# Kernel optimization log

Hardware: AMD Instinct MI355X
Metric: run time of the kernel (lower is better)

Reference implementation:

```python
import jax, jax.numpy as jnp
import numpy as np

STRIDES = (128, 64, 32, 16, 8)
FM_SHAPES = ((6, 10), (12, 20), (24, 40), (48, 80), (96, 160))
RATIOS = np.array([1.0, 2.0, 3.0])
BASE_SIZE = 4
POS_THR, NEG_THR, IGNORE = 0.5, 0.4, -1.0
ALPHA, GAMMA, SIGMA = 0.25, 2.0, 3.0


def _cell_anchors(stride):
    # classic generate_anchors: base 4x4 anchor, 3 aspect ratios, scale=stride
    w = h = float(BASE_SIZE)
    ctr = (BASE_SIZE - 1) / 2.0
    size = w * h
    ws = np.round(np.sqrt(size / RATIOS))
    hs = np.round(ws * RATIOS)
    a = np.stack([ctr - 0.5 * (ws - 1), ctr - 0.5 * (hs - 1),
                  ctr + 0.5 * (ws - 1), ctr + 0.5 * (hs - 1)], 1)
    aw = a[:, 2] - a[:, 0] + 1
    ah = a[:, 3] - a[:, 1] + 1
    cx = a[:, 0] + 0.5 * (aw - 1)
    cy = a[:, 1] + 0.5 * (ah - 1)
    sw = aw * stride
    sh = ah * stride
    return np.stack([cx - 0.5 * (sw - 1), cy - 0.5 * (sh - 1),
                     cx + 0.5 * (sw - 1), cy + 0.5 * (sh - 1)], 1)


def _all_anchors():
    outs = []
    for (h, w), s in zip(FM_SHAPES, STRIDES):
        cell = _cell_anchors(s)  # [3,4]
        sx = np.tile((np.arange(w) * s)[None, :], (h, 1)).reshape(-1)
        sy = np.tile((np.arange(h) * s)[:, None], (1, w)).reshape(-1)
        shifts = np.stack([sx, sy, sx, sy], 1)  # [h*w,4]
        outs.append((cell[None] + shifts[:, None]).reshape(-1, 4))
    return np.concatenate(outs, 0).astype(np.float32)  # [A,4]


def box_overlap(b, g):
    ab = (b[:, 2] - b[:, 0] + 1) * (b[:, 3] - b[:, 1] + 1)
    ag = (g[:, 2] - g[:, 0] + 1) * (g[:, 3] - g[:, 1] + 1)
    iw = jnp.clip(jnp.minimum(b[:, None, 2], g[None, :, 2]) - jnp.maximum(b[:, None, 0], g[None, :, 0]) + 1, 0)
    ih = jnp.clip(jnp.minimum(b[:, None, 3], g[None, :, 3]) - jnp.maximum(b[:, None, 1], g[None, :, 1]) + 1, 0)
    inter = iw * ih
    return inter / (ab[:, None] + ag[None, :] - inter)


def bbox_transform_inv(anc, dlt):
    w = anc[..., 2] - anc[..., 0] + 1
    h = anc[..., 3] - anc[..., 1] + 1
    cx = anc[..., 0] + 0.5 * (w - 1)
    cy = anc[..., 1] + 0.5 * (h - 1)
    mx = jnp.log(jnp.asarray(1000.0 / 16, dlt.dtype))
    pw = jnp.exp(jnp.minimum(dlt[..., 2], mx)) * w
    ph = jnp.exp(jnp.minimum(dlt[..., 3], mx)) * h
    pcx = dlt[..., 0] * w + cx
    pcy = dlt[..., 1] * h + cy
    return jnp.stack([pcx - 0.5 * (pw - 1), pcy - 0.5 * (ph - 1),
                      pcx + 0.5 * (pw - 1), pcy + 0.5 * (ph - 1)], -1)


def bbox_transform(anc, gt):
    aw = anc[..., 2] - anc[..., 0] + 1
    ah = anc[..., 3] - anc[..., 1] + 1
    acx = anc[..., 0] + 0.5 * (aw - 1)
    acy = anc[..., 1] + 0.5 * (ah - 1)
    gw = gt[..., 2] - gt[..., 0] + 1
    gh = gt[..., 3] - gt[..., 1] + 1
    gcx = gt[..., 0] + 0.5 * (gw - 1)
    gcy = gt[..., 1] + 0.5 * (gh - 1)
    return jnp.stack([(gcx - acx) / aw, (gcy - acy) / ah,
                      jnp.log(gw / aw), jnp.log(gh / ah)], -1)


def conv3x3(x, w, b):
    y = jax.lax.conv_general_dilated(x, w, (1, 1), 'SAME',
                                     dimension_numbers=('NCHW', 'OIHW', 'NCHW'))
    return y + b[None, :, None, None]


def _head(feat, cls_w, cls_b, box_w, box_b, score_w, score_b,
          bpred_w, bpred_b, iou_w, iou_b, num_w, num_b):
    n = feat.shape[0]
    c = feat
    for i in range(4):
        c = jax.nn.relu(conv3x3(c, cls_w[i], cls_b[i]))
    cls_prob = jax.nn.sigmoid(conv3x3(c, score_w, score_b))
    num_prob = conv3x3(c, num_w, num_b)
    r = feat
    for i in range(4):
        r = jax.nn.relu(conv3x3(r, box_w[i], box_b[i]))
    offsets = conv3x3(r, bpred_w, bpred_b)
    iou_prob = conv3x3(r, iou_w, iou_b)
    rs = lambda t, ch: t.transpose(0, 2, 3, 1).reshape(n, -1, ch)
    return rs(cls_prob, 2), rs(num_prob, 2), rs(offsets, 8), rs(iou_prob, 2)


def _forward(feats, gt_boxes, im_info, cls_w, cls_b, box_w, box_b,
             score_w, score_b, bpred_w, bpred_b, iou_w, iou_b, num_w, num_b):
    outs = [_head(f, cls_w, cls_b, box_w, box_b, score_w, score_b,
                  bpred_w, bpred_b, iou_w, iou_b, num_w, num_b) for f in feats]
    cls_prob = jnp.concatenate([o[0] for o in outs], 1)  # [n,A,2]
    num_prob = jnp.concatenate([o[1] for o in outs], 1)  # [n,A,2]
    offsets = jnp.concatenate([o[2] for o in outs], 1)   # [n,A,8]
    iou_prob = jnp.concatenate([o[3] for o in outs], 1)  # [n,A,2]
    anchors = jnp.asarray(_all_anchors())                # [A,4]
    A = anchors.shape[0]
    n = cls_prob.shape[0]
    G = gt_boxes.shape[1]
    counts = im_info[:, 5]
    gidx = jnp.arange(G, dtype=jnp.float32)

    def anchor_target_one(gt, cnt):
        valid = (gidx < cnt) & (gt[:, 4] != IGNORE)
        ov = jnp.where(valid[None, :], box_overlap(anchors, gt[:, :4]), -1.0)
        top2, idx = jax.lax.top_k(ov, 2)  # [A,2]
        labels = jnp.where(top2 >= POS_THR, 1.0,
                           jnp.where(top2 < NEG_THR, 0.0, -1.0))
        tgt = bbox_transform(anchors[:, None, :], gt[idx, :4])  # [A,2,4]
        return labels, tgt.reshape(-1, 4)

    rpn_labels, target_boxes = jax.vmap(anchor_target_one)(gt_boxes, counts)
    rpn_labels = jax.lax.stop_gradient(rpn_labels)        # [n,A,2]
    target_boxes = jax.lax.stop_gradient(target_boxes)    # [n,2A,4]
    anchors2 = jnp.repeat(anchors, 2, axis=0)             # [2A,4] interleaved

    def iou_target_one(gt, cnt, off):
        dt = bbox_transform_inv(anchors2, off.reshape(-1, 4))  # [2A,4]
        keep = ((gidx < cnt) & (gt[:, 4] != IGNORE)).astype(dt.dtype)
        ov = box_overlap(dt, gt[:, :4]) * keep[None, :]        # [2A,G]
        ov = ov.reshape(A, 2, G)
        a, b = ov[:, 0], ov[:, 1]
        i1 = jnp.argmax(a, 1)
        av = jnp.take_along_axis(a, i1[:, None], 1)
        b = b.at[jnp.arange(A), i1].set(0.0)
        bv = jnp.max(b, 1, keepdims=True)
        return jnp.concatenate([av, bv], 1)                    # [A,2]

    ious_target = jax.lax.stop_gradient(
        jax.vmap(iou_target_one)(gt_boxes, counts, offsets))

    a, b = rpn_labels[..., 0], rpn_labels[..., 1]
    ignores = b - (a == 0).astype(b.dtype) * (b != 0).astype(b.dtype)
    labels = jnp.stack([a, ignores], 2).reshape(n, -1)     # [n,2A]

    # focal (sigmoid_cross_entropy_retina)
    p = cls_prob.reshape(n, -1, 1)                          # [n,2A,1]
    mask = (labels != IGNORE).astype(p.dtype)
    onehot = ((labels * mask) == 1).astype(p.dtype)[..., None]
    pos = (1 - p) ** GAMMA * onehot * jnp.log(p)
    neg = p ** GAMMA * (1 - onehot) * jnp.log(1 - p)
    npos = jnp.maximum((labels > 0).astype(p.dtype).sum(), 1.0)
    cls_loss = (-(ALPHA * pos + (1 - ALPHA) * neg).sum(-1) * mask).sum() / npos

    # smooth_l1_loss_retina (sigma=3)
    off4 = offsets.reshape(n, -1, 4)                        # [n,2A,4]
    diff = off4 - target_boxes
    ad = jnp.abs(diff)
    s2 = SIGMA * SIGMA
    sl1 = jnp.where(ad < 1.0 / s2, 0.5 * s2 * diff * diff, ad - 0.5 / s2)
    posm = (labels > 0).astype(off4.dtype)
    bbox_loss = (sl1.sum(-1) * posm).sum() / jnp.maximum(posm.sum(), 1.0)

    # iou_l1_loss
    lab2 = labels.reshape(n, -1, 2)                         # [n,A,2]
    ioumask = (lab2 > 0).astype(iou_prob.dtype)
    iou_loss = (jnp.abs(iou_prob.reshape(n, -1, 2) - ious_target) * ioumask).sum() \
        / jnp.maximum(ioumask.sum(), 1.0)

    # softmax_loss over num-per-anchor predictions
    nlabels = (lab2 > 0).sum(2).reshape(-1) - 1             # [n*A] in {-1,0,1}
    score = num_prob.reshape(-1, 2)
    logp = jax.nn.log_softmax(score, -1)
    nm = (nlabels != -1)
    vl = jnp.where(nm, nlabels, 0)
    nmf = nm.astype(score.dtype)
    num_loss = (-(jnp.take_along_axis(logp, vl[:, None], 1)[:, 0]) * nmf).sum() \
        / jnp.maximum(nmf.sum(), 1.0)

    return jnp.stack([cls_loss, 2.0 * bbox_loss, 2.0 * iou_loss, num_loss])


def setup_inputs() -> dict:
    key = jax.random.key(0)
    ks = jax.random.split(key, 24)
    n, G = 2, 32
    inp = {}
    for i, (h, w) in enumerate(FM_SHAPES):
        inp[f"feat_p{7 - i}"] = jax.random.normal(ks[i], (n, 256, h, w), jnp.float32) * 0.5
    x1 = jax.random.uniform(ks[5], (n, G), minval=0.0, maxval=900.0)
    y1 = jax.random.uniform(ks[6], (n, G), minval=0.0, maxval=500.0)
    bw = jax.random.uniform(ks[7], (n, G), minval=32.0, maxval=300.0)
    bh = jax.random.uniform(ks[8], (n, G), minval=32.0, maxval=300.0)
    inp["gt_boxes"] = jnp.stack([x1, y1, x1 + bw, y1 + bh, jnp.ones((n, G))], -1).astype(jnp.float32)
    inp["im_info"] = jnp.tile(jnp.array([[768., 1280., 1., 768., 1280., 24.]], jnp.float32), (n, 1))
    std = 0.01
    inp["cls_w"] = jax.random.normal(ks[9], (4, 256, 256, 3, 3), jnp.float32) * std
    inp["cls_b"] = jnp.zeros((4, 256), jnp.float32)
    inp["box_w"] = jax.random.normal(ks[10], (4, 256, 256, 3, 3), jnp.float32) * std
    inp["box_b"] = jnp.zeros((4, 256), jnp.float32)
    prior_bias = -float(np.log((1 - 0.01) / 0.01))
    inp["score_w"] = jax.random.normal(ks[11], (6, 256, 3, 3), jnp.float32) * std
    inp["score_b"] = jnp.full((6,), prior_bias, jnp.float32)
    inp["bpred_w"] = jax.random.normal(ks[12], (24, 256, 3, 3), jnp.float32) * std
    inp["bpred_b"] = jnp.zeros((24,), jnp.float32)
    inp["iou_w"] = jax.random.normal(ks[13], (6, 256, 3, 3), jnp.float32) * std
    inp["iou_b"] = jnp.zeros((6,), jnp.float32)
    inp["num_w"] = jax.random.normal(ks[14], (6, 256, 3, 3), jnp.float32) * std
    inp["num_b"] = jnp.zeros((6,), jnp.float32)
    return inp


def reference(feat_p7, feat_p6, feat_p5, feat_p4, feat_p3, gt_boxes, im_info,
              cls_w, cls_b, box_w, box_b, score_w, score_b, bpred_w, bpred_b,
              iou_w, iou_b, num_w, num_b):
    feats = [feat_p7, feat_p6, feat_p5, feat_p4, feat_p3]
    return _forward(feats, gt_boxes, im_info, cls_w, cls_b, box_w, box_b,
                    score_w, score_b, bpred_w, bpred_b, iou_w, iou_b, num_w, num_b)
```

## Files before the change

kernel.cpp:

```cpp
#include <hip/hip_runtime.h>
#include <math.h>

#define A_TOTAL 61380
#define NGT 32
#define PTOT 21472

typedef _Float16 f16;
typedef f16 f16x8 __attribute__((ext_vector_type(8)));
typedef float f32x4 __attribute__((ext_vector_type(4)));

__device__ __constant__ int LV_H[5]    = {6, 12, 24, 48, 96};
__device__ __constant__ int LV_W[5]    = {10, 20, 40, 80, 160};
__device__ __constant__ int LV_PB[5]   = {0, 96, 404, 1496, 5596};
__device__ __constant__ int LV_TX[5]   = {1, 2, 3, 5, 10};

__device__ __forceinline__ void get_tile8(int t, int& lv, int& y0, int& x0)
{
  int local;
  if (t >= 44)      { lv = 4; local = t - 44; }
  else if (t >= 14) { lv = 3; local = t - 14; }
  else if (t >= 5)  { lv = 2; local = t - 5; }
  else if (t >= 1)  { lv = 1; local = t - 1; }
  else              { lv = 0; local = 0; }
  int tX = LV_TX[lv];
  y0 = (local / tX) * 8;
  x0 = (local % tX) * 16;
}

__device__ __forceinline__ void get_tile16(int t, int& lv, int& y0, int& x0)
{
  int local;
  if (t >= 24)      { lv = 4; local = t - 24; }
  else if (t >= 9)  { lv = 3; local = t - 9; }
  else if (t >= 3)  { lv = 2; local = t - 3; }
  else if (t >= 1)  { lv = 1; local = t - 1; }
  else              { lv = 0; local = 0; }
  int tX = LV_TX[lv];
  y0 = (local / tX) * 16;
  x0 = (local % tX) * 16;
}

__device__ __forceinline__ int padded_off(int p)
{
  if (p >= 5100)      { int po = p - 5100; int y = po / 160, x = po - y * 160; return 5596 + (y + 1) * 162 + x + 1; }
  else if (p >= 1260) { int po = p - 1260; int y = po / 80,  x = po - y * 80;  return 1496 + (y + 1) * 82  + x + 1; }
  else if (p >= 300)  { int po = p - 300;  int y = po / 40,  x = po - y * 40;  return 404  + (y + 1) * 42  + x + 1; }
  else if (p >= 60)   { int po = p - 60;   int y = po / 20,  x = po - y * 20;  return 96   + (y + 1) * 22  + x + 1; }
  else                { int y = p / 10, x = p - y * 10;                         return (y + 1) * 12 + x + 1; }
}

__global__ __launch_bounds__(64) void zero_borders(f16* __restrict__ act)
{
  int e = blockIdx.x, b = blockIdx.y, z = blockIdx.z;
  int lv, e0;
  if (e >= 496)      { lv = 4; e0 = e - 496; }
  else if (e >= 236) { lv = 3; e0 = e - 236; }
  else if (e >= 104) { lv = 2; e0 = e - 104; }
  else if (e >= 36)  { lv = 1; e0 = e - 36; }
  else               { lv = 0; e0 = e; }
  int Hp = LV_H[lv] + 2, Wp = LV_W[lv] + 2;
  int y, x;
  if (e0 < Wp)          { y = 0;      x = e0; }
  else if (e0 < 2 * Wp) { y = Hp - 1; x = e0 - Wp; }
  else { int e2 = e0 - 2 * Wp; y = 1 + (e2 >> 1); x = (e2 & 1) ? (Wp - 1) : 0; }
  f16* dst = act + ((size_t)z * 2 * PTOT + (size_t)b * PTOT + LV_PB[lv] + y * Wp + x) * 256
           + threadIdx.x * 4;
  *(uint2*)dst = (uint2){0u, 0u};
}

__global__ __launch_bounds__(256) void feats_to_nhwc(
    const float* __restrict__ f0, const float* __restrict__ f1,
    const float* __restrict__ f2, const float* __restrict__ f3,
    const float* __restrict__ f4, f16* __restrict__ act)
{
  const int b = blockIdx.z;
  const int c0 = blockIdx.y * 32;
  const int p0 = blockIdx.x * 32;
  const int tx = threadIdx.x & 31, ty = threadIdx.x >> 5;
  __shared__ float tl[32][33];

  int p = p0 + tx;
  const float* src = f0; int po = 0;
  if (p >= 5100)      { src = f4; po = p - 5100; }
  else if (p >= 1260) { src = f3; po = p - 1260; }
  else if (p >= 300)  { src = f2; po = p - 300;  }
  else if (p >= 60)   { src = f1; po = p - 60;   }
  else                { src = f0; po = p;        }
  int HW = (p >= 5100) ? 15360 : (p >= 1260) ? 3840 : (p >= 300) ? 960 : (p >= 60) ? 240 : 60;

#pragma unroll
  for (int k = 0; k < 4; ++k) {
    int c = c0 + ty + k * 8;
    float v = 0.f;
    if (p < 20460) v = src[((size_t)b * 256 + c) * HW + po];
    tl[ty + k * 8][tx] = v;
  }
  __syncthreads();
#pragma unroll
  for (int k = 0; k < 4; ++k) {
    int pp = p0 + ty + k * 8;
    if (pp < 20460)
      act[((size_t)b * PTOT + padded_off(pp)) * 256 + c0 + tx] = (f16)tl[tx][ty + k * 8];
  }
}

__global__ __launch_bounds__(256) void prep_tower_w3(
    const float* __restrict__ cls_w, const float* __restrict__ box_w,
    f16* __restrict__ wT)
{
  int blk = blockIdx.x;
  int l = blk >> 8, co = blk & 255;
  const float* src = (l < 4 ? cls_w + (size_t)l * 589824
                            : box_w + (size_t)(l - 4) * 589824)
                   + (size_t)co * 2304;
  __shared__ f16 sm[2304];
  int t = threadIdx.x;
#pragma unroll
  for (int j = 0; j < 9; ++j) sm[t + j * 256] = (f16)src[t + j * 256];
  __syncthreads();
#pragma unroll
  for (int it = 0; it < 2; ++it) {
    int c = t + it * 256;
    if (c < 288) {
      int tap = c >> 5, s = c & 31;
      f16x8 v;
#pragma unroll
      for (int e = 0; e < 8; ++e) v[e] = sm[(s * 8 + e) * 9 + tap];
      *(f16x8*)(wT + ((((size_t)l * 9 + tap) * 32 + s) * 256 + co) * 8) = v;
    }
  }
}

__global__ void prep_head_w3(const float* __restrict__ sw, const float* __restrict__ nw,
                             const float* __restrict__ bw, const float* __restrict__ iw,
                             const float* __restrict__ sb, const float* __restrict__ nb2,
                             const float* __restrict__ bb, const float* __restrict__ ib,
                             f16* __restrict__ wH, float* __restrict__ hb)
{
  int idx = blockIdx.x * 256 + threadIdx.x;
  if (idx < 18432) {
    int p = idx / 9216, rem = idx - p * 9216;
    int tap = rem / 1024, rem2 = rem - tap * 1024;
    int s = rem2 >> 5, co = rem2 & 31;
    int C1 = p ? 24 : 6;
    const float* w1 = p ? bw : sw;
    const float* w2 = p ? iw : nw;
    f16x8 v;
#pragma unroll
    for (int e = 0; e < 8; ++e) {
      int ci = s * 8 + e;
      float x = 0.f;
      if (co < C1)          x = w1[((size_t)co * 256 + ci) * 9 + tap];
      else if (co < C1 + 6) x = w2[((size_t)(co - C1) * 256 + ci) * 9 + tap];
      v[e] = (f16)x;
    }
    *(f16x8*)(wH + (size_t)idx * 8) = v;
  }
  if (idx < 64) {
    int pp = idx >> 5, jj = idx & 31;
    int C1b = pp ? 24 : 6;
    const float* b1 = pp ? bb : sb;
    const float* b2 = pp ? ib : nb2;
    float bv = 0.f;
    if (jj < C1b)          bv = b1[jj];
    else if (jj < C1b + 6) bv = b2[jj - C1b];
    hb[idx] = bv;
  }
}

__global__ __launch_bounds__(256, 2) void conv_mfma_tower3(
    const f16* __restrict__ in_cls, f16* __restrict__ out_cls,
    const f16* __restrict__ in_box, f16* __restrict__ out_box,
    const f16* __restrict__ wT, const float* __restrict__ cls_b,
    const float* __restrict__ box_b, int layer)
{
  int lv, y0, x0;
  get_tile8(blockIdx.x, lv, y0, x0);
  const int H = LV_H[lv], W = LV_W[lv], Wp = W + 2, pbase = LV_PB[lv];
  const int b = blockIdx.y, tw = blockIdx.z;
  const f16* in  = tw ? in_box : in_cls;
  f16*       out = tw ? out_box : out_cls;
  const f16* wB = wT + (size_t)(tw * 4 + layer) * 2304 * 256;
  const float* bias = (tw ? box_b : cls_b) + layer * 256;

  const int tid = threadIdx.x;
  const int lane = tid & 63, wid = tid >> 6;
  const int m = lane & 15, q = lane >> 4;
  const int mrow = (wid & 1) * 4;
  const int ncol = (wid >> 1) * 128;

  f32x4 acc[4][8];
#pragma unroll
  for (int i = 0; i < 4; ++i)
#pragma unroll
    for (int j = 0; j < 8; ++j) acc[i][j] = (f32x4){0.f, 0.f, 0.f, 0.f};

  const f16* inb = in + (size_t)(b * PTOT + pbase) * 256;
  const f16* pA = inb + ((size_t)(y0 + mrow) * Wp + x0 + m) * 256 + q * 8;
  const f16* pB = wB + ((size_t)q * 256 + ncol + m) * 8;

  for (int cb = 0; cb < 8; ++cb) {
    const f16* pAc = pA + cb * 32;
    const f16* pBc = pB + (size_t)cb * 4 * 256 * 8;
#pragma unroll
    for (int tap = 0; tap < 9; ++tap) {
      const int ky = tap / 3, kx = tap - ky * 3;
      f16x8 af[4], bf[8];
#pragma unroll
      for (int mb = 0; mb < 4; ++mb)
        af[mb] = *(const f16x8*)(pAc + ((size_t)(mb + ky) * Wp + kx) * 256);
#pragma unroll
      for (int nb = 0; nb < 8; ++nb)
        bf[nb] = *(const f16x8*)(pBc + (size_t)tap * 65536 + nb * 128);
#pragma unroll
      for (int mb = 0; mb < 4; ++mb)
#pragma unroll
        for (int nb = 0; nb < 8; ++nb)
          acc[mb][nb] = __builtin_amdgcn_mfma_f32_16x16x32_f16(af[mb], bf[nb], acc[mb][nb], 0, 0, 0);
    }
  }

  f16* outb = out + (size_t)(b * PTOT + pbase) * 256;
#pragma unroll
  for (int mb = 0; mb < 4; ++mb) {
    int y = y0 + mrow + mb;
    if (y >= H) continue;
#pragma unroll
    for (int nb = 0; nb < 8; ++nb) {
      int co = ncol + nb * 16 + m;
      float bi = bias[co];
#pragma unroll
      for (int r = 0; r < 4; ++r) {
        int x = x0 + q * 4 + r;
        if (x < W) {
          float v = fmaxf(acc[mb][nb][r] + bi, 0.f);
          outb[((size_t)(y + 1) * Wp + x + 1) * 256 + co] = (f16)v;
        }
      }
    }
  }
}

__global__ __launch_bounds__(256) void conv_mfma_head3(
    const f16* __restrict__ in_cls, const f16* __restrict__ in_box,
    const f16* __restrict__ wH, const float* __restrict__ hb,
    float* __restrict__ cls_prob, float* __restrict__ num_prob,
    float* __restrict__ offsets, float* __restrict__ iou_prob)
{
  int lv, y0, x0;
  get_tile16(blockIdx.x, lv, y0, x0);
  const int H = LV_H[lv], W = LV_W[lv], Wp = W + 2, pbase = LV_PB[lv];
  const int b = blockIdx.y, z = blockIdx.z;
  const f16* in = z ? in_box : in_cls;
  const f16* wB = wH + (size_t)z * 2304 * 32;
  const float* hbz = hb + z * 32;
  float* o1 = z ? offsets : cls_prob;
  float* o2 = z ? iou_prob : num_prob;
  const int C1 = z ? 24 : 6, P1 = z ? 8 : 2, SIG = z ? 0 : 1;

  const int tid = threadIdx.x;
  const int lane = tid & 63, wid = tid >> 6;
  const int m = lane & 15, q = lane >> 4;

  f32x4 acc[4][2];
#pragma unroll
  for (int i = 0; i < 4; ++i) { acc[i][0] = (f32x4){0,0,0,0}; acc[i][1] = (f32x4){0,0,0,0}; }

  const f16* inb = in + (size_t)(b * PTOT + pbase) * 256;
  const f16* pA = inb + ((size_t)(y0 + wid * 4) * Wp + x0 + m) * 256 + q * 8;
  const f16* pB = wB + ((size_t)q * 32 + m) * 8;

  for (int cb = 0; cb < 8; ++cb) {
    const f16* pAc = pA + cb * 32;
    const f16* pBc = pB + (size_t)cb * 4 * 32 * 8;
#pragma unroll
    for (int tap = 0; tap < 9; ++tap) {
      const int ky = tap / 3, kx = tap - ky * 3;
      f16x8 af[4], bf[2];
#pragma unroll
      for (int mb = 0; mb < 4; ++mb)
        af[mb] = *(const f16x8*)(pAc + ((size_t)(mb + ky) * Wp + kx) * 256);
#pragma unroll
      for (int nb = 0; nb < 2; ++nb)
        bf[nb] = *(const f16x8*)(pBc + (size_t)tap * 8192 + nb * 128);
#pragma unroll
      for (int mb = 0; mb < 4; ++mb)
#pragma unroll
        for (int nb = 0; nb < 2; ++nb)
          acc[mb][nb] = __builtin_amdgcn_mfma_f32_16x16x32_f16(af[mb], bf[nb], acc[mb][nb], 0, 0, 0);
    }
  }

  const int ro = pbase * 0 + 0;
  const int robase = (lv == 0 ? 0 : lv == 1 ? 60 : lv == 2 ? 300 : lv == 3 ? 1260 : 5100) * 3;
#pragma unroll
  for (int mb = 0; mb < 4; ++mb) {
    int y = y0 + wid * 4 + mb;
    if (y >= H) continue;
#pragma unroll
    for (int nb = 0; nb < 2; ++nb) {
      int j = nb * 16 + m;
      if (j >= C1 + 6) continue;
      float bi = hbz[j];
#pragma unroll
      for (int r = 0; r < 4; ++r) {
        int x = x0 + q * 4 + r;
        if (x < W) {
          float v = acc[mb][nb][r] + bi;
          int row0 = robase + (y * W + x) * 3;
          if (j < C1) {
            if (SIG) v = 1.f / (1.f + expf(-v));
            int jd = j / P1;
            o1[((size_t)b * A_TOTAL + row0 + jd) * P1 + (j - jd * P1)] = v;
          } else {
            int jj = j - C1;
            o2[((size_t)b * A_TOTAL + row0 + (jj >> 1)) * 2 + (jj & 1)] = v;
          }
        }
      }
    }
  }
  (void)ro;
}

__global__ void gen_anchors(float* __restrict__ anchors, float* __restrict__ accum)
{
  int i = blockIdx.x * 256 + threadIdx.x;
  if (blockIdx.x == 0 && threadIdx.x < 8) accum[threadIdx.x] = 0.f;
  if (i >= A_TOTAL) return;
  int off, s, Wl;
  if (i >= 15300)     { off = 15300; s = 8;   Wl = 160; }
  else if (i >= 3780) { off = 3780;  s = 16;  Wl = 80;  }
  else if (i >= 900)  { off = 900;   s = 32;  Wl = 40;  }
  else if (i >= 180)  { off = 180;   s = 64;  Wl = 20;  }
  else                { off = 0;     s = 128; Wl = 10;  }
  int r = i - off;
  int cell = r / 3, a = r - cell * 3;
  int y = cell / Wl, x = cell - y * Wl;
  float wsv = (a == 0) ? 4.f : (a == 1) ? 3.f : 2.f;
  float hsv = (a == 0) ? 4.f : 6.f;
  float sw = wsv * (float)s, sh = hsv * (float)s;
  float cx = (float)(x * s) + 1.5f, cy = (float)(y * s) + 1.5f;
  anchors[i * 4 + 0] = cx - 0.5f * (sw - 1.f);
  anchors[i * 4 + 1] = cy - 0.5f * (sh - 1.f);
  anchors[i * 4 + 2] = cx + 0.5f * (sw - 1.f);
  anchors[i * 4 + 3] = cy + 0.5f * (sh - 1.f);
}

__global__ __launch_bounds__(256) void anchor_target(
    const float* __restrict__ anchors, const float* __restrict__ gt,
    const float* __restrict__ iminfo, float* __restrict__ rpn, float* __restrict__ tgt)
{
  int i = blockIdx.x * 256 + threadIdx.x;
  int b = blockIdx.y;
  if (i >= A_TOTAL) return;
  float cnt = iminfo[b * 6 + 5];
  float ax1 = anchors[i*4+0], ay1 = anchors[i*4+1], ax2 = anchors[i*4+2], ay2 = anchors[i*4+3];
  float aw = ax2 - ax1 + 1.f, ah = ay2 - ay1 + 1.f, ab = aw * ah;
  float v1 = -1e30f, v2 = -1e30f; int i1 = 0, i2 = 0;
  for (int g = 0; g < NGT; ++g) {
    const float* gp = gt + (b * NGT + g) * 5;
    float ov = -1.f;
    if ((float)g < cnt && gp[4] != -1.f) {
      float iw = fmaxf(fminf(ax2, gp[2]) - fmaxf(ax1, gp[0]) + 1.f, 0.f);
      float ih = fmaxf(fminf(ay2, gp[3]) - fmaxf(ay1, gp[1]) + 1.f, 0.f);
      float inter = iw * ih;
      float ag = (gp[2] - gp[0] + 1.f) * (gp[3] - gp[1] + 1.f);
      ov = inter / (ab + ag - inter);
    }
    if (ov > v1)      { v2 = v1; i2 = i1; v1 = ov; i1 = g; }
    else if (ov > v2) { v2 = ov; i2 = g; }
  }
  float l1 = (v1 >= 0.5f) ? 1.f : ((v1 < 0.4f) ? 0.f : -1.f);
  float l2 = (v2 >= 0.5f) ? 1.f : ((v2 < 0.4f) ? 0.f : -1.f);
  rpn[(b * A_TOTAL + i) * 2 + 0] = l1;
  rpn[(b * A_TOTAL + i) * 2 + 1] = l2;
  float acx = ax1 + 0.5f * (aw - 1.f), acy = ay1 + 0.5f * (ah - 1.f);
  int idx2[2] = {i1, i2};
#pragma unroll
  for (int k = 0; k < 2; ++k) {
    const float* gp = gt + (b * NGT + idx2[k]) * 5;
    float gw = gp[2] - gp[0] + 1.f, gh = gp[3] - gp[1] + 1.f;
    float gcx = gp[0] + 0.5f * (gw - 1.f), gcy = gp[1] + 0.5f * (gh - 1.f);
    float* o = tgt + ((size_t)(b * 2 * A_TOTAL) + i * 2 + k) * 4;
    o[0] = (gcx - acx) / aw;  o[1] = (gcy - acy) / ah;
    o[2] = logf(gw / aw);     o[3] = logf(gh / ah);
  }
}

__global__ __launch_bounds__(256) void iou_target(
    const float* __restrict__ anchors, const float* __restrict__ gt,
    const float* __restrict__ iminfo, const float* __restrict__ offsets,
    float* __restrict__ ioust)
{
  int i = blockIdx.x * 256 + threadIdx.x;
  int b = blockIdx.y;
  if (i >= A_TOTAL) return;
  float cnt = iminfo[b * 6 + 5];
  float ax1 = anchors[i*4+0], ay1 = anchors[i*4+1], ax2 = anchors[i*4+2], ay2 = anchors[i*4+3];
  float aw = ax2 - ax1 + 1.f, ah = ay2 - ay1 + 1.f;
  float acx = ax1 + 0.5f * (aw - 1.f), acy = ay1 + 0.5f * (ah - 1.f);
  const float mx = 4.135166556742356f;
  float bx[2][4];
#pragma unroll
  for (int k = 0; k < 2; ++k) {
    const float* d = offsets + ((size_t)(b * A_TOTAL) + i) * 8 + k * 4;
    float pw = expf(fminf(d[2], mx)) * aw;
    float ph = expf(fminf(d[3], mx)) * ah;
    float pcx = d[0] * aw + acx, pcy = d[1] * ah + acy;
    bx[k][0] = pcx - 0.5f * (pw - 1.f); bx[k][1] = pcy - 0.5f * (ph - 1.f);
    bx[k][2] = pcx + 0.5f * (pw - 1.f); bx[k][3] = pcy + 0.5f * (ph - 1.f);
  }
  float area0 = (bx[0][2]-bx[0][0]+1.f) * (bx[0][3]-bx[0][1]+1.f);
  float area1 = (bx[1][2]-bx[1][0]+1.f) * (bx[1][3]-bx[1][1]+1.f);
  float av = -1e30f; int i1 = 0;
  for (int g = 0; g < NGT; ++g) {
    const float* gp = gt + (b * NGT + g) * 5;
    float keep = ((float)g < cnt && gp[4] != -1.f) ? 1.f : 0.f;
    float ag = (gp[2] - gp[0] + 1.f) * (gp[3] - gp[1] + 1.f);
    float iw = fmaxf(fminf(bx[0][2], gp[2]) - fmaxf(bx[0][0], gp[0]) + 1.f, 0.f);
    float ih = fmaxf(fminf(bx[0][3], gp[3]) - fmaxf(bx[0][1], gp[1]) + 1.f, 0.f);
    float inter = iw * ih;
    float ov = inter / (area0 + ag - inter) * keep;
    if (ov > av) { av = ov; i1 = g; }
  }
  float bv = -1e30f;
  for (int g = 0; g < NGT; ++g) {
    float val = 0.f;
    if (g != i1) {
      const float* gp = gt + (b * NGT + g) * 5;
      float keep = ((float)g < cnt && gp[4] != -1.f) ? 1.f : 0.f;
      float ag = (gp[2] - gp[0] + 1.f) * (gp[3] - gp[1] + 1.f);
      float iw = fmaxf(fminf(bx[1][2], gp[2]) - fmaxf(bx[1][0], gp[0]) + 1.f, 0.f);
      float ih = fmaxf(fminf(bx[1][3], gp[3]) - fmaxf(bx[1][1], gp[1]) + 1.f, 0.f);
      float inter = iw * ih;
      val = inter / (area1 + ag - inter) * keep;
    }
    bv = fmaxf(bv, val);
  }
  ioust[(b * A_TOTAL + i) * 2 + 0] = av;
  ioust[(b * A_TOTAL + i) * 2 + 1] = bv;
}

__global__ __launch_bounds__(256) void loss_reduce(
    const float* __restrict__ cls_prob, const float* __restrict__ num_prob,
    const float* __restrict__ offsets,  const float* __restrict__ iou_prob,
    const float* __restrict__ rpn,      const float* __restrict__ tgt,
    const float* __restrict__ ioust,    float* __restrict__ accum)
{
  int i = blockIdx.x * 256 + threadIdx.x;
  int b = blockIdx.y;
  float cls_s = 0.f, npos = 0.f, bb_s = 0.f, iou_s = 0.f, num_s = 0.f, num_c = 0.f;
  float la = 0.f, ign = 0.f;
  if (i < A_TOTAL) {
    int base = b * A_TOTAL + i;
    la = rpn[base * 2 + 0];
    float lb = rpn[base * 2 + 1];
    ign = lb - ((la == 0.f && lb != 0.f) ? 1.f : 0.f);
    float lab2[2] = {la, ign};
#pragma unroll
    for (int j = 0; j < 2; ++j) {
      float l = lab2[j];
      float mask = (l != -1.f) ? 1.f : 0.f;
      bool oh = (l * mask) == 1.f;
      float p = cls_prob[base * 2 + j];
      float term = oh ? (0.25f * (1.f - p) * (1.f - p) * logf(p))
                      : (0.75f * p * p * logf(1.f - p));
      cls_s += -term * mask;
      if (l > 0.f) {
        npos += 1.f;
#pragma unroll
        for (int c = 0; c < 4; ++c) {
          float d = offsets[(size_t)base * 8 + j * 4 + c]
                  - tgt[((size_t)(b * 2 * A_TOTAL) + i * 2 + j) * 4 + c];
          float ad = fabsf(d);
          bb_s += (ad < 1.f / 9.f) ? (4.5f * d * d) : (ad - 0.5f / 9.f);
        }
        iou_s += fabsf(iou_prob[base * 2 + j] - ioust[base * 2 + j]);
      }
    }
    int nl = ((la > 0.f) ? 1 : 0) + ((ign > 0.f) ? 1 : 0) - 1;
    if (nl != -1) {
      float s0 = num_prob[base * 2], s1 = num_prob[base * 2 + 1];
      float mm = fmaxf(s0, s1);
      float lse = mm + logf(expf(s0 - mm) + expf(s1 - mm));
      num_s += lse - ((nl == 0) ? s0 : s1);
      num_c += 1.f;
    }
  }
  __shared__ float red[6][4];
  float vals[6] = {cls_s, npos, bb_s, iou_s, num_s, num_c};
  int lane = threadIdx.x & 63, wid = threadIdx.x >> 6;
#pragma unroll
  for (int qq = 0; qq < 6; ++qq) {
    float v = vals[qq];
#pragma unroll
    for (int o = 32; o > 0; o >>= 1) v += __shfl_down(v, o);
    if (lane == 0) red[qq][wid] = v;
  }
  __syncthreads();
  if (threadIdx.x < 6) {
    float s = red[threadIdx.x][0] + red[threadIdx.x][1] + red[threadIdx.x][2] + red[threadIdx.x][3];
    atomicAdd(&accum[threadIdx.x], s);
  }
}

__global__ void finalize_loss(const float* __restrict__ acc, float* __restrict__ out)
{
  float npos = fmaxf(acc[1], 1.f);
  out[0] = acc[0] / npos;
  out[1] = 2.f * acc[2] / npos;
  out[2] = 2.f * acc[3] / npos;
  out[3] = acc[4] / fmaxf(acc[5], 1.f);
}

extern "C" void kernel_launch(void* const* d_in, const int* in_sizes, int n_in,
                              void* d_out, int out_size, void* d_ws, size_t ws_size,
                              hipStream_t stream)
{
  (void)in_sizes; (void)n_in; (void)out_size; (void)ws_size;
  const float* feat[5];
  for (int i = 0; i < 5; ++i) feat[i] = (const float*)d_in[i];
  const float* gt      = (const float*)d_in[5];
  const float* iminfo  = (const float*)d_in[6];
  const float* cls_w   = (const float*)d_in[7];
  const float* cls_b   = (const float*)d_in[8];
  const float* box_w   = (const float*)d_in[9];
  const float* box_b   = (const float*)d_in[10];
  const float* score_w = (const float*)d_in[11];
  const float* score_b = (const float*)d_in[12];
  const float* bpred_w = (const float*)d_in[13];
  const float* bpred_b = (const float*)d_in[14];
  const float* iou_w   = (const float*)d_in[15];
  const float* iou_b   = (const float*)d_in[16];
  const float* num_w   = (const float*)d_in[17];
  const float* num_b   = (const float*)d_in[18];

  const size_t ACT2 = (size_t)2 * PTOT * 256;
  f16* actF = (f16*)d_ws;
  f16* actA = actF + ACT2;
  f16* actB = actA + ACT2;
  f16* actC = actB + ACT2;
  f16* wT   = actC + ACT2;
  f16* wH   = wT + (size_t)8 * 2304 * 256;
  float* hb = (float*)(wH + (size_t)2 * 2304 * 32);

  float* cls_prob = (float*)actA;
  float* num_prob = cls_prob + 2 * A_TOTAL * 2;
  float* offsets  = num_prob + 2 * A_TOTAL * 2;
  float* iou_prob = offsets + 2 * A_TOTAL * 8;
  float* anchors  = iou_prob + 2 * A_TOTAL * 2;
  float* rpn      = anchors + A_TOTAL * 4;
  float* tgt      = rpn + 2 * A_TOTAL * 2;
  float* ioust    = tgt + 2 * 2 * A_TOTAL * 4;
  float* accum    = ioust + 2 * A_TOTAL * 2;

  prep_tower_w3<<<dim3(2048), 256, 0, stream>>>(cls_w, box_w, wT);
  prep_head_w3<<<dim3(72), 256, 0, stream>>>(
      score_w, num_w, bpred_w, iou_w, score_b, num_b, bpred_b, iou_b, wH, hb);
  zero_borders<<<dim3(1012, 2, 4), 64, 0, stream>>>(actF);
  feats_to_nhwc<<<dim3(640, 8, 2), 256, 0, stream>>>(
      feat[0], feat[1], feat[2], feat[3], feat[4], actF);

  dim3 tg(164, 2, 2);
  conv_mfma_tower3<<<tg, 256, 0, stream>>>(actF, actA, actF, actC, wT, cls_b, box_b, 0);
  conv_mfma_tower3<<<tg, 256, 0, stream>>>(actA, actB, actC, actF, wT, cls_b, box_b, 1);
  conv_mfma_tower3<<<tg, 256, 0, stream>>>(actB, actA, actF, actC, wT, cls_b, box_b, 2);
  conv_mfma_tower3<<<tg, 256, 0, stream>>>(actA, actB, actC, actF, wT, cls_b, box_b, 3);

  conv_mfma_head3<<<dim3(84, 2, 2), 256, 0, stream>>>(
      actB, actF, wH, hb, cls_prob, num_prob, offsets, iou_prob);

  dim3 agrid((A_TOTAL + 255) / 256, 2);
  gen_anchors<<<dim3((A_TOTAL + 255) / 256), 256, 0, stream>>>(anchors, accum);
  anchor_target<<<agrid, 256, 0, stream>>>(anchors, gt, iminfo, rpn, tgt);
  iou_target<<<agrid, 256, 0, stream>>>(anchors, gt, iminfo, offsets, ioust);
  loss_reduce<<<agrid, 256, 0, stream>>>(cls_prob, num_prob, offsets, iou_prob,
                                         rpn, tgt, ioust, accum);
  finalize_loss<<<1, 1, 0, stream>>>(accum, (float*)d_out);
}
```

Baseline: 842.0 us.

## Stage tower conv weights in LDS and split output channels across blocks

The tower conv kernel now splits the 256 output channels into two groups of 128 along the grid z dimension, which doubles the number of blocks and halves the accumulators per thread. For each 32-channel input block, 8 of the 9 taps of weights are copied into 64KB of shared memory with direct global-to-LDS loads and then read from LDS. The 9th tap is still read from global memory. This is meant to cut redundant global and L2 weight traffic across waves and to raise occupancy. In exchange it adds two barriers per channel block, re-reads the A activations twice as often, and the large LDS buffer may limit how many blocks fit per CU.

```diff
diff --git a/kernel.cpp b/kernel.cpp
--- a/kernel.cpp
+++ b/kernel.cpp
@@ -13,6 +13,12 @@
 __device__ __constant__ int LV_W[5]    = {10, 20, 40, 80, 160};
 __device__ __constant__ int LV_PB[5]   = {0, 96, 404, 1496, 5596};
 __device__ __constant__ int LV_TX[5]   = {1, 2, 3, 5, 10};
+
+typedef __attribute__((address_space(1))) const void* gptr_t;
+typedef __attribute__((address_space(3))) void* lptr_t;
+__device__ __forceinline__ void cp16_g2l(const void* g, void* l) {
+  __builtin_amdgcn_global_load_lds((gptr_t)g, (lptr_t)l, 16, 0, 0);
+}
 
 __device__ __forceinline__ void get_tile8(int t, int& lv, int& y0, int& x0)
 {
@@ -168,7 +174,7 @@
   }
 }
 
-__global__ __launch_bounds__(256, 2) void conv_mfma_tower3(
+__global__ __launch_bounds__(256, 2) void conv_mfma_tower4(
     const f16* __restrict__ in_cls, f16* __restrict__ out_cls,
     const f16* __restrict__ in_box, f16* __restrict__ out_box,
     const f16* __restrict__ wT, const float* __restrict__ cls_b,
@@ -177,7 +183,8 @@
   int lv, y0, x0;
   get_tile8(blockIdx.x, lv, y0, x0);
   const int H = LV_H[lv], W = LV_W[lv], Wp = W + 2, pbase = LV_PB[lv];
-  const int b = blockIdx.y, tw = blockIdx.z;
+  const int b = blockIdx.y;
+  const int z = blockIdx.z, tw = z >> 1, cog = z & 1;
   const f16* in  = tw ? in_box : in_cls;
   f16*       out = tw ? out_box : out_cls;
   const f16* wB = wT + (size_t)(tw * 4 + layer) * 2304 * 256;
@@ -187,35 +194,51 @@
   const int lane = tid & 63, wid = tid >> 6;
   const int m = lane & 15, q = lane >> 4;
   const int mrow = (wid & 1) * 4;
-  const int ncol = (wid >> 1) * 128;
-
-  f32x4 acc[4][8];
+  const int ncol = (wid >> 1) * 64;
+
+  __shared__ __align__(16) f16 Bs[4096 * 8];
+
+  f32x4 acc[4][4];
 #pragma unroll
   for (int i = 0; i < 4; ++i)
 #pragma unroll
-    for (int j = 0; j < 8; ++j) acc[i][j] = (f32x4){0.f, 0.f, 0.f, 0.f};
+    for (int j = 0; j < 4; ++j) acc[i][j] = (f32x4){0.f, 0.f, 0.f, 0.f};
 
   const f16* inb = in + (size_t)(b * PTOT + pbase) * 256;
   const f16* pA = inb + ((size_t)(y0 + mrow) * Wp + x0 + m) * 256 + q * 8;
-  const f16* pB = wB + ((size_t)q * 256 + ncol + m) * 8;
 
   for (int cb = 0; cb < 8; ++cb) {
+    __syncthreads();
+#pragma unroll
+    for (int it = 0; it < 16; ++it) {
+      int u = tid + it * 256;
+      int tap = u >> 9, r = u & 511;
+      int s = r >> 7, c = r & 127;
+      cp16_g2l(wB + (((size_t)(tap * 32 + cb * 4 + s)) * 256 + cog * 128 + c) * 8,
+               Bs + (size_t)u * 8);
+    }
+    __syncthreads();
     const f16* pAc = pA + cb * 32;
-    const f16* pBc = pB + (size_t)cb * 4 * 256 * 8;
 #pragma unroll
     for (int tap = 0; tap < 9; ++tap) {
       const int ky = tap / 3, kx = tap - ky * 3;
-      f16x8 af[4], bf[8];
+      f16x8 af[4], bf[4];
 #pragma unroll
       for (int mb = 0; mb < 4; ++mb)
         af[mb] = *(const f16x8*)(pAc + ((size_t)(mb + ky) * Wp + kx) * 256);
-#pragma unroll
-      for (int nb = 0; nb < 8; ++nb)
-        bf[nb] = *(const f16x8*)(pBc + (size_t)tap * 65536 + nb * 128);
+      if (tap < 8) {
+#pragma unroll
+        for (int nb = 0; nb < 4; ++nb)
+          bf[nb] = *(const f16x8*)(Bs + (size_t)(tap * 512 + q * 128 + ncol + nb * 16 + m) * 8);
+      } else {
+#pragma unroll
+        for (int nb = 0; nb < 4; ++nb)
+          bf[nb] = *(const f16x8*)(wB + (((size_t)(256 + cb * 4 + q)) * 256 + cog * 128 + ncol + nb * 16 + m) * 8);
+      }
 #pragma unroll
       for (int mb = 0; mb < 4; ++mb)
 #pragma unroll
-        for (int nb = 0; nb < 8; ++nb)
+        for (int nb = 0; nb < 4; ++nb)
           acc[mb][nb] = __builtin_amdgcn_mfma_f32_16x16x32_f16(af[mb], bf[nb], acc[mb][nb], 0, 0, 0);
     }
   }
@@ -226,8 +249,8 @@
     int y = y0 + mrow + mb;
     if (y >= H) continue;
 #pragma unroll
-    for (int nb = 0; nb < 8; ++nb) {
-      int co = ncol + nb * 16 + m;
+    for (int nb = 0; nb < 4; ++nb) {
+      int co = cog * 128 + ncol + nb * 16 + m;
       float bi = bias[co];
 #pragma unroll
       for (int r = 0; r < 4; ++r) {
@@ -291,7 +314,6 @@
     }
   }
 
-  const int ro = pbase * 0 + 0;
   const int robase = (lv == 0 ? 0 : lv == 1 ? 60 : lv == 2 ? 300 : lv == 3 ? 1260 : 5100) * 3;
 #pragma unroll
   for (int mb = 0; mb < 4; ++mb) {
@@ -320,7 +342,6 @@
       }
     }
   }
-  (void)ro;
 }
 
 __global__ void gen_anchors(float* __restrict__ anchors, float* __restrict__ accum)
@@ -562,11 +583,11 @@
   feats_to_nhwc<<<dim3(640, 8, 2), 256, 0, stream>>>(
       feat[0], feat[1], feat[2], feat[3], feat[4], actF);
 
-  dim3 tg(164, 2, 2);
-  conv_mfma_tower3<<<tg, 256, 0, stream>>>(actF, actA, actF, actC, wT, cls_b, box_b, 0);
-  conv_mfma_tower3<<<tg, 256, 0, stream>>>(actA, actB, actC, actF, wT, cls_b, box_b, 1);
-  conv_mfma_tower3<<<tg, 256, 0, stream>>>(actB, actA, actF, actC, wT, cls_b, box_b, 2);
-  conv_mfma_tower3<<<tg, 256, 0, stream>>>(actA, actB, actC, actF, wT, cls_b, box_b, 3);
+  dim3 tg(164, 2, 4);
+  conv_mfma_tower4<<<tg, 256, 0, stream>>>(actF, actA, actF, actC, wT, cls_b, box_b, 0);
+  conv_mfma_tower4<<<tg, 256, 0, stream>>>(actA, actB, actC, actF, wT, cls_b, box_b, 1);
+  conv_mfma_tower4<<<tg, 256, 0, stream>>>(actB, actA, actF, actC, wT, cls_b, box_b, 2);
+  conv_mfma_tower4<<<tg, 256, 0, stream>>>(actA, actB, actC, actF, wT, cls_b, box_b, 3);
 
   conv_mfma_head3<<<dim3(84, 2, 2), 256, 0, stream>>>(
       actB, actF, wH, hb, cls_prob, num_prob, offsets, iou_prob);
```

New measurement: 902.2 us. 7.2% more time.
